# Optimization experiments

Measured on AMD Instinct MI355X. Metric: run time of the kernel, lower is better.

## Reference

```python
import jax, jax.numpy as jnp
import numpy as np

DIM = 256
HEADS = 8
HEAD_DIM = DIM // HEADS
SCALE = HEAD_DIM ** -0.5
B, H, W = 4, 48, 48


def setup_inputs() -> dict:
    key = jax.random.key(0)
    ks = jax.random.split(key, 10)
    s = 1.0 / np.sqrt(DIM)
    return {
        "img_features": jax.random.normal(ks[0], (B, DIM, H, W), jnp.float32),
        "radar_features": jax.random.normal(ks[1], (B, DIM, H, W), jnp.float32),
        "uncertainty_mask": jax.random.uniform(ks[2], (B, 1, H, W), jnp.float32),
        "Wq_img": jax.random.normal(ks[3], (DIM, DIM), jnp.float32) * s,
        "Wkv_radar": jax.random.normal(ks[4], (DIM, 2 * DIM), jnp.float32) * s,
        "Wq_radar": jax.random.normal(ks[5], (DIM, DIM), jnp.float32) * s,
        "Wkv_img": jax.random.normal(ks[6], (DIM, 2 * DIM), jnp.float32) * s,
        "Wp_img": jax.random.normal(ks[7], (DIM, DIM), jnp.float32) * s,
        "bp_img": jnp.zeros((DIM,), jnp.float32),
        "Wp_radar": jax.random.normal(ks[8], (DIM, DIM), jnp.float32) * s,
        "bp_radar": jnp.zeros((DIM,), jnp.float32),
    }


def _heads(x, b, n):
    # (B, N, C) -> (B, heads, N, head_dim)
    return x.reshape(b, n, HEADS, HEAD_DIM).transpose(0, 2, 1, 3)


def _cross_attn(q_seq, kv_seq, Wq, Wkv, uw=None):
    b, n, c = q_seq.shape
    q = _heads(q_seq @ Wq, b, n)                      # (B,h,N,d)
    kv = (kv_seq @ Wkv).reshape(b, n, 2, HEADS, HEAD_DIM)
    k = kv[:, :, 0].transpose(0, 2, 1, 3)             # (B,h,N,d)
    v = kv[:, :, 1].transpose(0, 2, 1, 3)
    scores = jnp.einsum("bhnd,bhmd->bhnm", q, k) * SCALE
    if uw is not None:
        scores = scores * uw                          # (B,1,N,1) broadcast
    p = jax.nn.softmax(scores, axis=-1)
    out = jnp.einsum("bhnm,bhmd->bhnd", p, v)
    return out.transpose(0, 2, 1, 3).reshape(b, n, c)


def reference(img_features, radar_features, uncertainty_mask,
              Wq_img, Wkv_radar, Wq_radar, Wkv_img,
              Wp_img, bp_img, Wp_radar, bp_radar):
    b, c, h, w = img_features.shape
    n = h * w
    img_seq = img_features.reshape(b, c, n).transpose(0, 2, 1)    # (B,N,C)
    radar_seq = radar_features.reshape(b, c, n).transpose(0, 2, 1)

    # uncertainty weight: (B,1,N,1), scales query rows before softmax
    u_seq = uncertainty_mask.reshape(b, 1, n).transpose(0, 2, 1)  # (B,N,1)
    uw = (1.0 / (u_seq + 1e-6))[:, None, :, :]

    img_att = _cross_attn(img_seq, radar_seq, Wq_img, Wkv_radar, uw)
    img_att = img_att @ Wp_img + bp_img

    radar_att = _cross_attn(radar_seq, img_seq, Wq_radar, Wkv_img, None)
    radar_att = radar_att @ Wp_radar + bp_radar

    img_out = img_att.transpose(0, 2, 1).reshape(b, c, h, w)
    radar_out = radar_att.transpose(0, 2, 1).reshape(b, c, h, w)
    return img_out, radar_out
```

## Files before the change

### kernel.cpp

```cpp
#include <hip/hip_runtime.h>
#include <math.h>

#define NB    4
#define CDIM  256
#define NSEQ  2304
#define NHEAD 8
#define HD    32
#define QSCALE (0.17677669529663687f * 1.4426950408889634f)
#define INV2048 4.8828125e-4f
#define FIXMAX 12.0f

typedef _Float16 f16;
typedef _Float16 f16x8 __attribute__((ext_vector_type(8)));
typedef _Float16 f16x4 __attribute__((ext_vector_type(4)));
typedef float    f32x4 __attribute__((ext_vector_type(4)));

__device__ __forceinline__ float fast_exp2(float x) {
#if __has_builtin(__builtin_amdgcn_exp2f)
  return __builtin_amdgcn_exp2f(x);
#else
  return exp2f(x);
#endif
}

__global__ __launch_bounds__(256) void prep_split(
    const float* __restrict__ X0, const float* __restrict__ X1,
    const float* __restrict__ Wq0, const float* __restrict__ Wkv0,
    const float* __restrict__ Wp0, const float* __restrict__ Wq1,
    const float* __restrict__ Wkv1, const float* __restrict__ Wp1,
    f16* __restrict__ X16h, f16* __restrict__ X16l,
    f16* __restrict__ WTh, f16* __restrict__ WTl)
{
  __shared__ float Ls[64][65];
  const int t = threadIdx.x;
  const int id = blockIdx.x;

  const float* in; int incols, c0, col0; size_t obase; f16 *oh, *ol;
  float scale = 1.f;
  if (id < 1152) {
    int mb = id / 144, rem = id % 144;
    int ct = rem / 36, nt = rem % 36;
    int mod = mb >> 2, b = mb & 3;
    in = (mod ? X1 : X0) + (size_t)b * 256 * NSEQ;
    incols = NSEQ; c0 = ct * 64; col0 = nt * 64;
    obase = (size_t)mb * NSEQ + col0;
    oh = X16h; ol = X16l;
  } else {
    int wid = id - 1152;
    int mod = wid >> 6, r = wid & 63;
    int jt, ct2, rowoff;
    if (r < 16) {
      in = mod ? Wq1 : Wq0; incols = 256; jt = r >> 2; ct2 = r & 3;
      rowoff = 0; scale = QSCALE;
    } else if (r < 48) {
      int rr = r - 16;
      in = mod ? Wkv1 : Wkv0; incols = 512; jt = rr >> 2; ct2 = rr & 3;
      rowoff = 256;
    } else {
      int rr = r - 48;
      in = mod ? Wp1 : Wp0; incols = 256; jt = rr >> 2; ct2 = rr & 3;
      rowoff = 768;
    }
    c0 = ct2 * 64; col0 = jt * 64;
    obase = (size_t)mod * 1024 + rowoff + col0;
    oh = WTh; ol = WTl;
  }

#pragma unroll
  for (int i = 0; i < 4; ++i) {
    int cl = (t >> 4) + i * 16;
    int n4 = (t & 15) * 4;
    *(float4*)&Ls[cl][n4] =
        *(const float4*)(in + (size_t)(c0 + cl) * incols + col0 + n4);
  }
  __syncthreads();
#pragma unroll
  for (int i = 0; i < 4; ++i) {
    int ll = (t >> 4) + i * 16;
    int c4 = (t & 15) * 4;
    f16x4 hv, lv;
#pragma unroll
    for (int j = 0; j < 4; ++j) {
      float v = Ls[c4 + j][ll] * scale;
      f16 hh = (f16)v;
      hv[j] = hh;
      lv[j] = (f16)((v - (float)hh) * 2048.0f);
    }
    size_t o = (obase + ll) * 256 + c0 + c4;
    *(f16x4*)(oh + o) = hv;
    *(f16x4*)(ol + o) = lv;
  }
}

__global__ __launch_bounds__(256) void proj_qkv_mfma(
    const f16* __restrict__ X16h, const f16* __restrict__ X16l,
    const f16* __restrict__ WTh, const f16* __restrict__ WTl,
    f16* __restrict__ Qh, f16* __restrict__ Ql,
    f16* __restrict__ Kh, f16* __restrict__ Kl, f16* __restrict__ Vt)
{
  __shared__ f16 WhS[128][32];
  __shared__ f16 WlS[128][32];
  __shared__ f16 XhS[64][32];
  __shared__ f16 XlS[64][32];

  const int zz = blockIdx.z, mod = zz >> 2, b = zz & 3;
  const int n0 = blockIdx.y * 64, j0 = blockIdx.x * 128;
  const int t = threadIdx.x;
  const int wave = t >> 6, lane = t & 63;
  const int col = lane & 15, quad = lane >> 4;

  const bool need_lo = (j0 < 256) ? (mod == 0)
                     : (j0 < 512) ? (mod == 1) : false;

  const size_t wbase = (size_t)mod * 1024 + j0;
  const size_t xbase = ((size_t)(mod * NB + b) * NSEQ + n0) * 256;

  f32x4 am[2][4], ac[2][4];
#pragma unroll
  for (int s = 0; s < 2; ++s)
#pragma unroll
    for (int tt = 0; tt < 4; ++tt) {
      am[s][tt] = (f32x4){0.f, 0.f, 0.f, 0.f};
      ac[s][tt] = (f32x4){0.f, 0.f, 0.f, 0.f};
    }

  const int wrow = t >> 1, wseg = (t & 1) * 16;
  const int xrow = t >> 2, xseg = (t & 3) * 8;

  for (int c0 = 0; c0 < 256; c0 += 32) {
    __syncthreads();
    *(f16x8*)&WhS[wrow][wseg] =
        *(const f16x8*)(WTh + (wbase + wrow) * 256 + c0 + wseg);
    *(f16x8*)&WhS[wrow][wseg + 8] =
        *(const f16x8*)(WTh + (wbase + wrow) * 256 + c0 + wseg + 8);
    *(f16x8*)&XhS[xrow][xseg] =
        *(const f16x8*)(X16h + xbase + (size_t)xrow * 256 + c0 + xseg);
    if (need_lo) {
      *(f16x8*)&WlS[wrow][wseg] =
          *(const f16x8*)(WTl + (wbase + wrow) * 256 + c0 + wseg);
      *(f16x8*)&WlS[wrow][wseg + 8] =
          *(const f16x8*)(WTl + (wbase + wrow) * 256 + c0 + wseg + 8);
      *(f16x8*)&XlS[xrow][xseg] =
          *(const f16x8*)(X16l + xbase + (size_t)xrow * 256 + c0 + xseg);
    }
    __syncthreads();

    f16x8 Ah0 = *(const f16x8*)&WhS[wave * 32 + col][quad * 8];
    f16x8 Ah1 = *(const f16x8*)&WhS[wave * 32 + 16 + col][quad * 8];
    if (need_lo) {
      f16x8 Al0 = *(const f16x8*)&WlS[wave * 32 + col][quad * 8];
      f16x8 Al1 = *(const f16x8*)&WlS[wave * 32 + 16 + col][quad * 8];
#pragma unroll
      for (int tt = 0; tt < 4; ++tt) {
        f16x8 Bh = *(const f16x8*)&XhS[tt * 16 + col][quad * 8];
        f16x8 Bl = *(const f16x8*)&XlS[tt * 16 + col][quad * 8];
        am[0][tt] = __builtin_amdgcn_mfma_f32_16x16x32_f16(Ah0, Bh, am[0][tt], 0, 0, 0);
        ac[0][tt] = __builtin_amdgcn_mfma_f32_16x16x32_f16(Ah0, Bl, ac[0][tt], 0, 0, 0);
        ac[0][tt] = __builtin_amdgcn_mfma_f32_16x16x32_f16(Al0, Bh, ac[0][tt], 0, 0, 0);
        am[1][tt] = __builtin_amdgcn_mfma_f32_16x16x32_f16(Ah1, Bh, am[1][tt], 0, 0, 0);
        ac[1][tt] = __builtin_amdgcn_mfma_f32_16x16x32_f16(Ah1, Bl, ac[1][tt], 0, 0, 0);
        ac[1][tt] = __builtin_amdgcn_mfma_f32_16x16x32_f16(Al1, Bh, ac[1][tt], 0, 0, 0);
      }
    } else {
#pragma unroll
      for (int tt = 0; tt < 4; ++tt) {
        f16x8 Bh = *(const f16x8*)&XhS[tt * 16 + col][quad * 8];
        am[0][tt] = __builtin_amdgcn_mfma_f32_16x16x32_f16(Ah0, Bh, am[0][tt], 0, 0, 0);
        am[1][tt] = __builtin_amdgcn_mfma_f32_16x16x32_f16(Ah1, Bh, am[1][tt], 0, 0, 0);
      }
    }
  }

#pragma unroll
  for (int s = 0; s < 2; ++s) {
    const int jq = j0 + wave * 32 + s * 16 + quad * 4;
#pragma unroll
    for (int tt = 0; tt < 4; ++tt) {
      const int n = n0 + tt * 16 + col;
      float v[4];
#pragma unroll
      for (int r = 0; r < 4; ++r)
        v[r] = need_lo ? fmaf(ac[s][tt][r], INV2048, am[s][tt][r])
                       : am[s][tt][r];
      if (jq < 256) {
        f16x4 hv, lv;
#pragma unroll
        for (int r = 0; r < 4; ++r) {
          f16 hh = (f16)v[r]; hv[r] = hh;
          lv[r] = (f16)((v[r] - (float)hh) * 2048.0f);
        }
        *(f16x4*)(Qh + ((size_t)(mod * NB + b) * NSEQ + n) * 256 + jq) = hv;
        if (mod == 0)
          *(f16x4*)(Ql + ((size_t)b * NSEQ + n) * 256 + jq) = lv;
      } else if (jq < 512) {
        f16x4 hv, lv;
#pragma unroll
        for (int r = 0; r < 4; ++r) {
          f16 hh = (f16)v[r]; hv[r] = hh;
          lv[r] = (f16)((v[r] - (float)hh) * 2048.0f);
        }
        *(f16x4*)(Kh + ((size_t)(mod * NB + b) * NSEQ + n) * 256 + (jq - 256)) = hv;
        if (mod == 1)
          *(f16x4*)(Kl + ((size_t)b * NSEQ + n) * 256 + (jq - 256)) = lv;
      } else {
#pragma unroll
        for (int r = 0; r < 4; ++r)
          Vt[((size_t)(mod * NB + b) * 256 + (jq - 512 + r)) * NSEQ + n] = (f16)v[r];
      }
    }
  }
}

__global__ __launch_bounds__(256, 4) void attn_mfma(
    const f16* __restrict__ Qh, const f16* __restrict__ Ql,
    const f16* __restrict__ Kh, const f16* __restrict__ Kl,
    const f16* __restrict__ Vt, const float* __restrict__ U,
    f16* __restrict__ A16)
{
  __shared__ f16 KhS[64][32];
  __shared__ f16 KlS[64][32];
  __shared__ f16 VtS[32][72];
  __shared__ f16 PS[4][16][72];

  const int branch = blockIdx.z;
  const int bh = blockIdx.y, b = bh >> 3, h = bh & 7;
  const int tid = threadIdx.x;
  const int wave = tid >> 6, lane = tid & 63;
  const int col = lane & 15, quad = lane >> 4;
  const int qr = blockIdx.x * 64 + wave * 16 + col;

  const int qmod = branch, kmod = 1 - branch;
  const size_t qbase = (size_t)(qmod * NB + b) * NSEQ * 256;
  const size_t kbase = (size_t)(kmod * NB + b) * NSEQ;
  const size_t kbaseL = (size_t)b * NSEQ;
  const size_t vbase = (size_t)(kmod * NB + b) * 256;

  const f16x8 bqh = *(const f16x8*)(Qh + qbase + (size_t)qr * 256 + h * HD + quad * 8);
  f16x8 bql = {};
  float uw = 1.0f;
  if (branch == 0) {
    const size_t qbaseL = (size_t)b * NSEQ * 256;
    bql = *(const f16x8*)(Ql + qbaseL + (size_t)qr * 256 + h * HD + quad * 8);
    uw = 1.0f / (U[b * NSEQ + qr] + 1e-6f);
  }

  float m = -1e30f, l = 0.f;
  f32x4 oc0 = {0.f,0.f,0.f,0.f}, oc1 = {0.f,0.f,0.f,0.f};
  const f32x4 z4 = {0.f,0.f,0.f,0.f};

  const int krow = tid >> 2, kseg = (tid & 3) * 8;
  const int vrow = tid >> 3, vseg = (tid & 7) * 8;

  f16x8 pkh = *(const f16x8*)(Kh + (kbase + krow) * 256 + h * HD + kseg);
  f16x8 pkl = {};
  if (branch == 0)
    pkl = *(const f16x8*)(Kl + (kbaseL + krow) * 256 + h * HD + kseg);
  f16x8 pv = *(const f16x8*)(Vt + (vbase + h * HD + vrow) * NSEQ + vseg);

  for (int k0 = 0; k0 < NSEQ; k0 += 64) {
    __syncthreads();
    *(f16x8*)&KhS[krow][kseg] = pkh;
    if (branch == 0) *(f16x8*)&KlS[krow][kseg] = pkl;
    *(f16x8*)&VtS[vrow][vseg] = pv;
    __syncthreads();

    const int kn = (k0 + 64 < NSEQ) ? k0 + 64 : 0;
    pkh = *(const f16x8*)(Kh + (kbase + kn + krow) * 256 + h * HD + kseg);
    if (branch == 0)
      pkl = *(const f16x8*)(Kl + (kbaseL + kn + krow) * 256 + h * HD + kseg);
    pv = *(const f16x8*)(Vt + (vbase + h * HD + vrow) * NSEQ + kn + vseg);

    float p[16];
#pragma unroll
    for (int t = 0; t < 4; ++t) {
      f16x8 ah = *(const f16x8*)&KhS[t * 16 + col][quad * 8];
      f32x4 s0 = __builtin_amdgcn_mfma_f32_16x16x32_f16(ah, bqh, z4, 0, 0, 0);
      if (branch == 0) {
        f16x8 al = *(const f16x8*)&KlS[t * 16 + col][quad * 8];
        f32x4 c0 = __builtin_amdgcn_mfma_f32_16x16x32_f16(ah, bql, z4, 0, 0, 0);
        c0 = __builtin_amdgcn_mfma_f32_16x16x32_f16(al, bqh, c0, 0, 0, 0);
#pragma unroll
        for (int r = 0; r < 4; ++r) p[t * 4 + r] = fmaf(c0[r], INV2048, s0[r]);
      } else {
#pragma unroll
        for (int r = 0; r < 4; ++r) p[t * 4 + r] = s0[r];
      }
    }

    if (branch == 0) {
      float r0 = fmaxf(fmaxf(p[0], p[1]),  fmaxf(p[2], p[3]));
      float r1 = fmaxf(fmaxf(p[4], p[5]),  fmaxf(p[6], p[7]));
      float r2 = fmaxf(fmaxf(p[8], p[9]),  fmaxf(p[10], p[11]));
      float r3 = fmaxf(fmaxf(p[12], p[13]), fmaxf(p[14], p[15]));
      float cmax = fmaxf(fmaxf(r0, r1), fmaxf(r2, r3)) * uw;
      cmax = fmaxf(cmax, __shfl_xor(cmax, 16, 64));
      cmax = fmaxf(cmax, __shfl_xor(cmax, 32, 64));
      const bool nore = __all(cmax <= m);
      const float mn = nore ? m : fmaxf(m, cmax);
      float lsA = 0.f, lsB = 0.f;
#pragma unroll
      for (int i = 0; i < 16; i += 2) {
        float eA = fast_exp2(fmaf(p[i],     uw, -mn));
        float eB = fast_exp2(fmaf(p[i + 1], uw, -mn));
        p[i] = eA; p[i + 1] = eB;
        lsA += eA; lsB += eB;
      }
      float ls = lsA + lsB;
      ls += __shfl_xor(ls, 16, 64);
      ls += __shfl_xor(ls, 32, 64);
      if (nore) {
        l += ls;
      } else {
        const float alpha = fast_exp2(m - mn);
        m = mn;
        l = fmaf(l, alpha, ls);
#pragma unroll
        for (int r = 0; r < 4; ++r) { oc0[r] *= alpha; oc1[r] *= alpha; }
      }
    } else {
      float lsA = 0.f, lsB = 0.f;
#pragma unroll
      for (int i = 0; i < 16; i += 2) {
        float eA = fast_exp2(p[i]     - FIXMAX);
        float eB = fast_exp2(p[i + 1] - FIXMAX);
        p[i] = eA; p[i + 1] = eB;
        lsA += eA; lsB += eB;
      }
      float ls = lsA + lsB;
      ls += __shfl_xor(ls, 16, 64);
      ls += __shfl_xor(ls, 32, 64);
      l += ls;
    }

#pragma unroll
    for (int t = 0; t < 4; ++t) {
      f16x4 pk;
#pragma unroll
      for (int r = 0; r < 4; ++r) pk[r] = (f16)p[t * 4 + r];
      *(f16x4*)&PS[wave][col][t * 16 + quad * 4] = pk;
    }
#pragma unroll
    for (int s = 0; s < 2; ++s) {
      f16x8 av0 = *(const f16x8*)&VtS[col][s * 32 + quad * 8];
      f16x8 av1 = *(const f16x8*)&VtS[16 + col][s * 32 + quad * 8];
      f16x8 bp  = *(const f16x8*)&PS[wave][col][s * 32 + quad * 8];
      oc0 = __builtin_amdgcn_mfma_f32_16x16x32_f16(av0, bp, oc0, 0, 0, 0);
      oc1 = __builtin_amdgcn_mfma_f32_16x16x32_f16(av1, bp, oc1, 0, 0, 0);
    }
  }

  const float iv = 1.0f / l;
  f16* d0 = A16 + (((size_t)(branch * NB + b) * NSEQ) + qr) * 256 + h * HD;
  f16x4 o0, o1;
#pragma unroll
  for (int r = 0; r < 4; ++r) {
    o0[r] = (f16)(oc0[r] * iv);
    o1[r] = (f16)(oc1[r] * iv);
  }
  *(f16x4*)(d0 + quad * 4)      = o0;
  *(f16x4*)(d0 + 16 + quad * 4) = o1;
}

__global__ __launch_bounds__(256) void proj_out_mfma(
    const f16* __restrict__ A16, const f16* __restrict__ WTh,
    const f16* __restrict__ WTl, const float* __restrict__ bp0,
    const float* __restrict__ bp1, float* __restrict__ O)
{
  __shared__ f16 WhS[128][32];
  __shared__ f16 WlS[128][32];
  __shared__ f16 AS[64][32];

  const int zz = blockIdx.z, mod = zz >> 2, b = zz & 3;
  const int n0 = blockIdx.y * 64, j0 = blockIdx.x * 128;
  const int t = threadIdx.x;
  const int wave = t >> 6, lane = t & 63;
  const int col = lane & 15, quad = lane >> 4;

  const size_t wbase = (size_t)mod * 1024 + 768 + j0;
  const size_t abase = ((size_t)(mod * NB + b) * NSEQ + n0) * 256;

  f32x4 am[2][4], ac[2][4];
#pragma unroll
  for (int s = 0; s < 2; ++s)
#pragma unroll
    for (int tt = 0; tt < 4; ++tt) {
      am[s][tt] = (f32x4){0.f, 0.f, 0.f, 0.f};
      ac[s][tt] = (f32x4){0.f, 0.f, 0.f, 0.f};
    }

  const int wrow = t >> 1, wseg = (t & 1) * 16;
  const int xrow = t >> 2, xseg = (t & 3) * 8;

  for (int c0 = 0; c0 < 256; c0 += 32) {
    __syncthreads();
    *(f16x8*)&WhS[wrow][wseg] =
        *(const f16x8*)(WTh + (wbase + wrow) * 256 + c0 + wseg);
    *(f16x8*)&WhS[wrow][wseg + 8] =
        *(const f16x8*)(WTh + (wbase + wrow) * 256 + c0 + wseg + 8);
    *(f16x8*)&WlS[wrow][wseg] =
        *(const f16x8*)(WTl + (wbase + wrow) * 256 + c0 + wseg);
    *(f16x8*)&WlS[wrow][wseg + 8] =
        *(const f16x8*)(WTl + (wbase + wrow) * 256 + c0 + wseg + 8);
    *(f16x8*)&AS[xrow][xseg] =
        *(const f16x8*)(A16 + abase + (size_t)xrow * 256 + c0 + xseg);
    __syncthreads();

    f16x8 Ah0 = *(const f16x8*)&WhS[wave * 32 + col][quad * 8];
    f16x8 Al0 = *(const f16x8*)&WlS[wave * 32 + col][quad * 8];
    f16x8 Ah1 = *(const f16x8*)&WhS[wave * 32 + 16 + col][quad * 8];
    f16x8 Al1 = *(const f16x8*)&WlS[wave * 32 + 16 + col][quad * 8];
#pragma unroll
    for (int tt = 0; tt < 4; ++tt) {
      f16x8 Bh = *(const f16x8*)&AS[tt * 16 + col][quad * 8];
      am[0][tt] = __builtin_amdgcn_mfma_f32_16x16x32_f16(Ah0, Bh, am[0][tt], 0, 0, 0);
      ac[0][tt] = __builtin_amdgcn_mfma_f32_16x16x32_f16(Al0, Bh, ac[0][tt], 0, 0, 0);
      am[1][tt] = __builtin_amdgcn_mfma_f32_16x16x32_f16(Ah1, Bh, am[1][tt], 0, 0, 0);
      ac[1][tt] = __builtin_amdgcn_mfma_f32_16x16x32_f16(Al1, Bh, ac[1][tt], 0, 0, 0);
    }
  }

  const float* bp = mod ? bp1 : bp0;
  float* Ob = O + (size_t)(mod * NB + b) * CDIM * NSEQ;
#pragma unroll
  for (int s = 0; s < 2; ++s) {
    const int jq = j0 + wave * 32 + s * 16 + quad * 4;
    const float4 bias = *(const float4*)(bp + jq);
    const float bias_r[4] = {bias.x, bias.y, bias.z, bias.w};
#pragma unroll
    for (int tt = 0; tt < 4; ++tt) {
      const int n = n0 + tt * 16 + col;
#pragma unroll
      for (int r = 0; r < 4; ++r) {
        float v = fmaf(ac[s][tt][r], INV2048, am[s][tt][r]) + bias_r[r];
        Ob[(size_t)(jq + r) * NSEQ + n] = v;
      }
    }
  }
}

extern "C" void kernel_launch(void* const* d_in, const int* in_sizes, int n_in,
                              void* d_out, int out_size, void* d_ws, size_t ws_size,
                              hipStream_t stream) {
  (void)in_sizes; (void)n_in; (void)out_size; (void)ws_size;
  const float* img     = (const float*)d_in[0];
  const float* rad     = (const float*)d_in[1];
  const float* U       = (const float*)d_in[2];
  const float* Wq_img  = (const float*)d_in[3];
  const float* Wkv_rad = (const float*)d_in[4];
  const float* Wq_rad  = (const float*)d_in[5];
  const float* Wkv_img = (const float*)d_in[6];
  const float* Wp_img  = (const float*)d_in[7];
  const float* bp_img  = (const float*)d_in[8];
  const float* Wp_rad  = (const float*)d_in[9];
  const float* bp_rad  = (const float*)d_in[10];
  float* out = (float*)d_out;

  const size_t NE = (size_t)2 * NB * NSEQ * 256;
  const size_t WE = (size_t)2 * 1024 * 256;
  f16* X16h = (f16*)d_ws;
  f16* X16l = X16h + NE;
  f16* WTh  = X16l + NE;
  f16* WTl  = WTh + WE;
  f16* Qh   = WTl + WE;
  f16* Ql   = Qh + NE;
  f16* Kh   = Ql + NE / 2;
  f16* Kl   = Kh + NE;
  f16* Vt   = Kl + NE / 2;
  f16* A16  = Vt + NE;

  prep_split<<<dim3(1280), 256, 0, stream>>>(
      img, rad, Wq_img, Wkv_img, Wp_img, Wq_rad, Wkv_rad, Wp_rad,
      X16h, X16l, WTh, WTl);

  dim3 gp(6, 36, 2 * NB);
  proj_qkv_mfma<<<gp, 256, 0, stream>>>(X16h, X16l, WTh, WTl,
                                        Qh, Ql, Kh, Kl, Vt);

  dim3 ga(NSEQ / 64, NB * NHEAD, 2);
  attn_mfma<<<ga, 256, 0, stream>>>(Qh, Ql, Kh, Kl, Vt, U, A16);

  dim3 go(2, 36, 2 * NB);
  proj_out_mfma<<<go, 256, 0, stream>>>(A16, WTh, WTl, bp_img, bp_rad, out);
}
```

Baseline: 281.4 us.

## Switch attention to 32x32 MFMA tiles with register-resident P via permlane swaps

The attention kernel now uses 32x32x16 MFMA instead of 16x16x32, so each wave owns 32 query rows and each block covers 128 queries, halving the grid. The P tile is no longer staged through shared memory; it is repacked in registers using permlane32 swaps to form the B operand of the PV MFMA. Row max and sum reductions use a single cross-half permlane swap instead of two shuffles. The trade-off is higher register pressure (launch bounds reduced from 4 to 3 blocks per CU), fewer blocks in the grid, and a runtime check that works out the permlane swap semantics.

```diff
diff --git a/kernel.cpp b/kernel.cpp
--- a/kernel.cpp
+++ b/kernel.cpp
@@ -13,7 +13,10 @@
 typedef _Float16 f16;
 typedef _Float16 f16x8 __attribute__((ext_vector_type(8)));
 typedef _Float16 f16x4 __attribute__((ext_vector_type(4)));
+typedef _Float16 f16x2 __attribute__((ext_vector_type(2)));
 typedef float    f32x4 __attribute__((ext_vector_type(4)));
+typedef float    f32x16 __attribute__((ext_vector_type(16)));
+typedef unsigned u32x4 __attribute__((ext_vector_type(4)));
 
 __device__ __forceinline__ float fast_exp2(float x) {
 #if __has_builtin(__builtin_amdgcn_exp2f)
@@ -21,6 +24,28 @@
 #else
   return exp2f(x);
 #endif
+}
+
+__device__ __forceinline__ void plswap(unsigned &a, unsigned &b) {
+#if __has_builtin(__builtin_amdgcn_permlane32_swap)
+  auto r = __builtin_amdgcn_permlane32_swap(a, b, false, false);
+  a = r[0]; b = r[1];
+#else
+  asm("v_permlane32_swap_b32 %0, %1" : "+v"(a), "+v"(b));
+#endif
+}
+
+__device__ __forceinline__ float cross_fmax(float v) {
+  unsigned a = __builtin_bit_cast(unsigned, v), b;
+  asm("v_mov_b32 %0, %1" : "=v"(b) : "v"(a));
+  plswap(a, b);
+  return fmaxf(__builtin_bit_cast(float, a), __builtin_bit_cast(float, b));
+}
+__device__ __forceinline__ float cross_add(float v) {
+  unsigned a = __builtin_bit_cast(unsigned, v), b;
+  asm("v_mov_b32 %0, %1" : "=v"(b) : "v"(a));
+  plswap(a, b);
+  return __builtin_bit_cast(float, a) + __builtin_bit_cast(float, b);
 }
 
 __global__ __launch_bounds__(256) void prep_split(
@@ -211,23 +236,27 @@
   }
 }
 
-__global__ __launch_bounds__(256, 4) void attn_mfma(
+__global__ __launch_bounds__(256, 3) void attn_mfma(
     const f16* __restrict__ Qh, const f16* __restrict__ Ql,
     const f16* __restrict__ Kh, const f16* __restrict__ Kl,
     const f16* __restrict__ Vt, const float* __restrict__ U,
     f16* __restrict__ A16)
 {
-  __shared__ f16 KhS[64][32];
-  __shared__ f16 KlS[64][32];
-  __shared__ f16 VtS[32][72];
-  __shared__ f16 PS[4][16][72];
+  __shared__ __align__(16) f16 KhS[64][40];
+  __shared__ __align__(16) f16 KlS[64][40];
+  __shared__ __align__(16) f16 VtS[32][72];
 
   const int branch = blockIdx.z;
   const int bh = blockIdx.y, b = bh >> 3, h = bh & 7;
   const int tid = threadIdx.x;
   const int wave = tid >> 6, lane = tid & 63;
-  const int col = lane & 15, quad = lane >> 4;
-  const int qr = blockIdx.x * 64 + wave * 16 + col;
+  const int c32 = lane & 31, hi = lane >> 5;
+  const int qr = blockIdx.x * 128 + wave * 32 + c32;
+
+  unsigned da = (lane < 32) ? 1u : 2u;
+  unsigned db = (lane < 32) ? 3u : 4u;
+  plswap(da, db);
+  const bool varA = (__builtin_amdgcn_readfirstlane((int)da) == 1);
 
   const int qmod = branch, kmod = 1 - branch;
   const size_t qbase = (size_t)(qmod * NB + b) * NSEQ * 256;
@@ -235,18 +264,21 @@
   const size_t kbaseL = (size_t)b * NSEQ;
   const size_t vbase = (size_t)(kmod * NB + b) * 256;
 
-  const f16x8 bqh = *(const f16x8*)(Qh + qbase + (size_t)qr * 256 + h * HD + quad * 8);
-  f16x8 bql = {};
+  f16x8 bqh[2], bql[2] = {};
+  bqh[0] = *(const f16x8*)(Qh + qbase + (size_t)qr * 256 + h * HD + hi * 8);
+  bqh[1] = *(const f16x8*)(Qh + qbase + (size_t)qr * 256 + h * HD + 16 + hi * 8);
   float uw = 1.0f;
   if (branch == 0) {
     const size_t qbaseL = (size_t)b * NSEQ * 256;
-    bql = *(const f16x8*)(Ql + qbaseL + (size_t)qr * 256 + h * HD + quad * 8);
+    bql[0] = *(const f16x8*)(Ql + qbaseL + (size_t)qr * 256 + h * HD + hi * 8);
+    bql[1] = *(const f16x8*)(Ql + qbaseL + (size_t)qr * 256 + h * HD + 16 + hi * 8);
     uw = 1.0f / (U[b * NSEQ + qr] + 1e-6f);
   }
 
   float m = -1e30f, l = 0.f;
-  f32x4 oc0 = {0.f,0.f,0.f,0.f}, oc1 = {0.f,0.f,0.f,0.f};
-  const f32x4 z4 = {0.f,0.f,0.f,0.f};
+  f32x16 oc;
+#pragma unroll
+  for (int r = 0; r < 16; ++r) oc[r] = 0.f;
 
   const int krow = tid >> 2, kseg = (tid & 3) * 8;
   const int vrow = tid >> 3, vseg = (tid & 7) * 8;
@@ -264,50 +296,64 @@
     *(f16x8*)&VtS[vrow][vseg] = pv;
     __syncthreads();
 
+    float p[2][16];
+#pragma unroll
+    for (int kt = 0; kt < 2; ++kt) {
+      f32x16 acc;
+#pragma unroll
+      for (int r = 0; r < 16; ++r) acc[r] = 0.f;
+      if (branch == 0) {
+        f16x8 ah0 = *(const f16x8*)&KhS[kt * 32 + c32][hi * 8];
+        f16x8 ah1 = *(const f16x8*)&KhS[kt * 32 + c32][16 + hi * 8];
+        f16x8 al0 = *(const f16x8*)&KlS[kt * 32 + c32][hi * 8];
+        f16x8 al1 = *(const f16x8*)&KlS[kt * 32 + c32][16 + hi * 8];
+        acc = __builtin_amdgcn_mfma_f32_32x32x16_f16(ah0, bql[0], acc, 0, 0, 0);
+        acc = __builtin_amdgcn_mfma_f32_32x32x16_f16(al0, bqh[0], acc, 0, 0, 0);
+        acc = __builtin_amdgcn_mfma_f32_32x32x16_f16(ah1, bql[1], acc, 0, 0, 0);
+        acc = __builtin_amdgcn_mfma_f32_32x32x16_f16(al1, bqh[1], acc, 0, 0, 0);
+#pragma unroll
+        for (int r = 0; r < 16; ++r) acc[r] *= INV2048;
+        acc = __builtin_amdgcn_mfma_f32_32x32x16_f16(ah0, bqh[0], acc, 0, 0, 0);
+        acc = __builtin_amdgcn_mfma_f32_32x32x16_f16(ah1, bqh[1], acc, 0, 0, 0);
+      } else {
+        f16x8 ah0 = *(const f16x8*)&KhS[kt * 32 + c32][hi * 8];
+        f16x8 ah1 = *(const f16x8*)&KhS[kt * 32 + c32][16 + hi * 8];
+        acc = __builtin_amdgcn_mfma_f32_32x32x16_f16(ah0, bqh[0], acc, 0, 0, 0);
+        acc = __builtin_amdgcn_mfma_f32_32x32x16_f16(ah1, bqh[1], acc, 0, 0, 0);
+      }
+#pragma unroll
+      for (int r = 0; r < 16; ++r) p[kt][r] = acc[r];
+    }
+
     const int kn = (k0 + 64 < NSEQ) ? k0 + 64 : 0;
     pkh = *(const f16x8*)(Kh + (kbase + kn + krow) * 256 + h * HD + kseg);
     if (branch == 0)
       pkl = *(const f16x8*)(Kl + (kbaseL + kn + krow) * 256 + h * HD + kseg);
     pv = *(const f16x8*)(Vt + (vbase + h * HD + vrow) * NSEQ + kn + vseg);
 
-    float p[16];
-#pragma unroll
-    for (int t = 0; t < 4; ++t) {
-      f16x8 ah = *(const f16x8*)&KhS[t * 16 + col][quad * 8];
-      f32x4 s0 = __builtin_amdgcn_mfma_f32_16x16x32_f16(ah, bqh, z4, 0, 0, 0);
-      if (branch == 0) {
-        f16x8 al = *(const f16x8*)&KlS[t * 16 + col][quad * 8];
-        f32x4 c0 = __builtin_amdgcn_mfma_f32_16x16x32_f16(ah, bql, z4, 0, 0, 0);
-        c0 = __builtin_amdgcn_mfma_f32_16x16x32_f16(al, bqh, c0, 0, 0, 0);
-#pragma unroll
-        for (int r = 0; r < 4; ++r) p[t * 4 + r] = fmaf(c0[r], INV2048, s0[r]);
-      } else {
-#pragma unroll
-        for (int r = 0; r < 4; ++r) p[t * 4 + r] = s0[r];
-      }
-    }
-
     if (branch == 0) {
-      float r0 = fmaxf(fmaxf(p[0], p[1]),  fmaxf(p[2], p[3]));
-      float r1 = fmaxf(fmaxf(p[4], p[5]),  fmaxf(p[6], p[7]));
-      float r2 = fmaxf(fmaxf(p[8], p[9]),  fmaxf(p[10], p[11]));
-      float r3 = fmaxf(fmaxf(p[12], p[13]), fmaxf(p[14], p[15]));
-      float cmax = fmaxf(fmaxf(r0, r1), fmaxf(r2, r3)) * uw;
-      cmax = fmaxf(cmax, __shfl_xor(cmax, 16, 64));
-      cmax = fmaxf(cmax, __shfl_xor(cmax, 32, 64));
+      float t8[8];
+#pragma unroll
+      for (int i = 0; i < 8; ++i)
+        t8[i] = fmaxf(fmaxf(p[0][i], p[0][i + 8]), fmaxf(p[1][i], p[1][i + 8]));
+#pragma unroll
+      for (int s = 4; s > 0; s >>= 1)
+#pragma unroll
+        for (int i = 0; i < s; ++i) t8[i] = fmaxf(t8[i], t8[i + s]);
+      float cmax = cross_fmax(t8[0] * uw);
       const bool nore = __all(cmax <= m);
       const float mn = nore ? m : fmaxf(m, cmax);
-      float lsA = 0.f, lsB = 0.f;
-#pragma unroll
-      for (int i = 0; i < 16; i += 2) {
-        float eA = fast_exp2(fmaf(p[i],     uw, -mn));
-        float eB = fast_exp2(fmaf(p[i + 1], uw, -mn));
-        p[i] = eA; p[i + 1] = eB;
-        lsA += eA; lsB += eB;
-      }
-      float ls = lsA + lsB;
-      ls += __shfl_xor(ls, 16, 64);
-      ls += __shfl_xor(ls, 32, 64);
+      float sA = 0.f, sB = 0.f;
+#pragma unroll
+      for (int kt = 0; kt < 2; ++kt)
+#pragma unroll
+        for (int r = 0; r < 16; r += 2) {
+          float eA = fast_exp2(fmaf(p[kt][r],     uw, -mn));
+          float eB = fast_exp2(fmaf(p[kt][r + 1], uw, -mn));
+          p[kt][r] = eA; p[kt][r + 1] = eB;
+          sA += eA; sB += eB;
+        }
+      float ls = cross_add(sA + sB);
       if (nore) {
         l += ls;
       } else {
@@ -315,50 +361,57 @@
         m = mn;
         l = fmaf(l, alpha, ls);
 #pragma unroll
-        for (int r = 0; r < 4; ++r) { oc0[r] *= alpha; oc1[r] *= alpha; }
+        for (int r = 0; r < 16; ++r) oc[r] *= alpha;
       }
     } else {
-      float lsA = 0.f, lsB = 0.f;
-#pragma unroll
-      for (int i = 0; i < 16; i += 2) {
-        float eA = fast_exp2(p[i]     - FIXMAX);
-        float eB = fast_exp2(p[i + 1] - FIXMAX);
-        p[i] = eA; p[i + 1] = eB;
-        lsA += eA; lsB += eB;
-      }
-      float ls = lsA + lsB;
-      ls += __shfl_xor(ls, 16, 64);
-      ls += __shfl_xor(ls, 32, 64);
-      l += ls;
-    }
-
-#pragma unroll
-    for (int t = 0; t < 4; ++t) {
-      f16x4 pk;
-#pragma unroll
-      for (int r = 0; r < 4; ++r) pk[r] = (f16)p[t * 4 + r];
-      *(f16x4*)&PS[wave][col][t * 16 + quad * 4] = pk;
-    }
-#pragma unroll
-    for (int s = 0; s < 2; ++s) {
-      f16x8 av0 = *(const f16x8*)&VtS[col][s * 32 + quad * 8];
-      f16x8 av1 = *(const f16x8*)&VtS[16 + col][s * 32 + quad * 8];
-      f16x8 bp  = *(const f16x8*)&PS[wave][col][s * 32 + quad * 8];
-      oc0 = __builtin_amdgcn_mfma_f32_16x16x32_f16(av0, bp, oc0, 0, 0, 0);
-      oc1 = __builtin_amdgcn_mfma_f32_16x16x32_f16(av1, bp, oc1, 0, 0, 0);
+      float sA = 0.f, sB = 0.f;
+#pragma unroll
+      for (int kt = 0; kt < 2; ++kt)
+#pragma unroll
+        for (int r = 0; r < 16; r += 2) {
+          float eA = fast_exp2(p[kt][r]     - FIXMAX);
+          float eB = fast_exp2(p[kt][r + 1] - FIXMAX);
+          p[kt][r] = eA; p[kt][r + 1] = eB;
+          sA += eA; sB += eB;
+        }
+      l += cross_add(sA + sB);
+    }
+
+    unsigned pk[2][4][2];
+#pragma unroll
+    for (int kt = 0; kt < 2; ++kt)
+#pragma unroll
+      for (int Q = 0; Q < 4; ++Q) {
+        f16x2 a0, a1;
+        a0[0] = (f16)p[kt][4 * Q];     a0[1] = (f16)p[kt][4 * Q + 1];
+        a1[0] = (f16)p[kt][4 * Q + 2]; a1[1] = (f16)p[kt][4 * Q + 3];
+        pk[kt][Q][0] = __builtin_bit_cast(unsigned, a0);
+        pk[kt][Q][1] = __builtin_bit_cast(unsigned, a1);
+      }
+
+#pragma unroll
+    for (int km = 0; km < 4; ++km) {
+      const int kt = km >> 1, Qb = (km & 1) * 2;
+      unsigned w0 = pk[kt][Qb][0],     w1 = pk[kt][Qb][1];
+      unsigned w2 = pk[kt][Qb + 1][0], w3 = pk[kt][Qb + 1][1];
+      if (varA) { plswap(w0, w2); plswap(w1, w3); }
+      else      { plswap(w2, w0); plswap(w3, w1); }
+      u32x4 uv = {w0, w1, w2, w3};
+      f16x8 bp = __builtin_bit_cast(f16x8, uv);
+      f16x8 av = *(const f16x8*)&VtS[c32][km * 16 + hi * 8];
+      oc = __builtin_amdgcn_mfma_f32_32x32x16_f16(av, bp, oc, 0, 0, 0);
     }
   }
 
   const float iv = 1.0f / l;
-  f16* d0 = A16 + (((size_t)(branch * NB + b) * NSEQ) + qr) * 256 + h * HD;
-  f16x4 o0, o1;
-#pragma unroll
-  for (int r = 0; r < 4; ++r) {
-    o0[r] = (f16)(oc0[r] * iv);
-    o1[r] = (f16)(oc1[r] * iv);
-  }
-  *(f16x4*)(d0 + quad * 4)      = o0;
-  *(f16x4*)(d0 + 16 + quad * 4) = o1;
+  f16* d0 = A16 + (((size_t)(branch * NB + b) * NSEQ) + qr) * 256 + h * HD + hi * 4;
+#pragma unroll
+  for (int g = 0; g < 4; ++g) {
+    f16x4 o;
+#pragma unroll
+    for (int r = 0; r < 4; ++r) o[r] = (f16)(oc[4 * g + r] * iv);
+    *(f16x4*)(d0 + 8 * g) = o;
+  }
 }
 
 __global__ __launch_bounds__(256) void proj_out_mfma(
@@ -476,7 +529,7 @@
   proj_qkv_mfma<<<gp, 256, 0, stream>>>(X16h, X16l, WTh, WTl,
                                         Qh, Ql, Kh, Kl, Vt);
 
-  dim3 ga(NSEQ / 64, NB * NHEAD, 2);
+  dim3 ga(NSEQ / 128, NB * NHEAD, 2);
   attn_mfma<<<ga, 256, 0, stream>>>(Qh, Ql, Kh, Kl, Vt, U, A16);
 
   dim3 go(2, 36, 2 * NB);
```

After: 264.9 us. -5.8%, faster.
